# Kernel tuning notes

Hardware: AMD Instinct MI355X
Metric: run time of the kernel (lower is better)

The kernel has to match this reference:

```python
import jax, jax.numpy as jnp
import numpy as np

N, E, G = 50000, 500000, 8
IN, HID, OUT, NC, H = 256, 128, 64, 10, 2
NPG = N // G  # nodes per graph
NEG_SLOPE = 0.2


def setup_inputs() -> dict:
    key = jax.random.key(0)
    ks = jax.random.split(key, 24)
    x = jax.random.normal(ks[0], (N, IN), jnp.float32)
    # edges constrained to stay within each graph, no self-loops
    src = jax.random.randint(ks[1], (E,), 0, N)
    base = (src // NPG) * NPG
    off = jax.random.randint(ks[2], (E,), 1, NPG)
    dst = base + (src - base + off) % NPG
    edge_index = jnp.stack([src, dst], axis=0).astype(jnp.int32)
    edge_attr = jax.random.uniform(ks[3], (E, 1), jnp.float32)
    batch = jnp.repeat(jnp.arange(G, dtype=jnp.int32), NPG)
    y = jax.random.randint(ks[4], (N,), 0, NC).astype(jnp.int32)

    s = 0.1
    p = {
        'W1': jax.random.normal(ks[5], (IN, H * HID), jnp.float32) * s,
        'att_src1': jax.random.normal(ks[6], (H, HID), jnp.float32) * s,
        'att_dst1': jax.random.normal(ks[7], (H, HID), jnp.float32) * s,
        'We1': jax.random.normal(ks[8], (1, H * HID), jnp.float32) * s,
        'att_edge1': jax.random.normal(ks[9], (H, HID), jnp.float32) * s,
        'b1': jnp.zeros((HID,), jnp.float32),
        'W2': jax.random.normal(ks[10], (HID, H * OUT), jnp.float32) * s,
        'att_src2': jax.random.normal(ks[11], (H, OUT), jnp.float32) * s,
        'att_dst2': jax.random.normal(ks[12], (H, OUT), jnp.float32) * s,
        'We2': jax.random.normal(ks[13], (1, H * OUT), jnp.float32) * s,
        'att_edge2': jax.random.normal(ks[14], (H, OUT), jnp.float32) * s,
        'b2': jnp.zeros((OUT,), jnp.float32),
        'Wc': jax.random.normal(ks[15], (OUT, NC), jnp.float32) * s,
        'bc': jnp.zeros((NC,), jnp.float32),
    }
    return dict(x=x, edge_index=edge_index, edge_attr=edge_attr, batch=batch, y=y, **p)


def _gat_layer(x, src, dst, eattr, W, a_src, a_dst, We, a_e, b, n_nodes, C):
    # PyG GATConv: heads=H, concat=False (mean over heads), edge_dim features.
    xp = (x @ W).reshape(n_nodes, H, C)                    # [N,H,C]
    al_s = jnp.einsum('nhc,hc->nh', xp, a_src)             # [N,H]
    al_d = jnp.einsum('nhc,hc->nh', xp, a_dst)
    ef = (eattr @ We).reshape(-1, H, C)                    # [E,H,C]
    al_e = jnp.einsum('ehc,hc->eh', ef, a_e)               # [E,H]
    alpha = jax.nn.leaky_relu(al_s[src] + al_d[dst] + al_e, NEG_SLOPE)
    # edge softmax grouped by destination (every dst has a self-loop -> no empty segs)
    m = jax.ops.segment_max(alpha, dst, num_segments=n_nodes)
    ex = jnp.exp(alpha - m[dst])
    denom = jax.ops.segment_sum(ex, dst, num_segments=n_nodes)
    w = ex / (denom[dst] + 1e-16)                          # [E,H]
    msg = xp[src] * w[:, :, None]                          # [E,H,C]
    out = jax.ops.segment_sum(msg, dst, num_segments=n_nodes)  # [N,H,C]
    return out.mean(axis=1) + b


def reference(x, edge_index, edge_attr, batch, y,
              W1, att_src1, att_dst1, We1, att_edge1, b1,
              W2, att_src2, att_dst2, We2, att_edge2, b2,
              Wc, bc):
    src, dst = edge_index[0], edge_index[1]
    # add self-loops; edge_attr fill = per-graph mean (as in the per-graph loop)
    g = batch[src]
    cnt = jax.ops.segment_sum(jnp.ones_like(edge_attr[:, 0]), g, num_segments=G)
    mean_attr = jax.ops.segment_sum(edge_attr, g, num_segments=G) / cnt[:, None]
    loop_attr = mean_attr[batch]                           # [N,1]
    ar = jnp.arange(N, dtype=src.dtype)
    src_a = jnp.concatenate([src, ar])
    dst_a = jnp.concatenate([dst, ar])
    ea = jnp.concatenate([edge_attr, loop_attr], axis=0)

    h = _gat_layer(x, src_a, dst_a, ea, W1, att_src1, att_dst1, We1, att_edge1, b1, N, HID)
    h = jax.nn.relu(h)
    h = _gat_layer(h, src_a, dst_a, ea, W2, att_src2, att_dst2, We2, att_edge2, b2, N, OUT)
    pred = h @ Wc + bc                                     # [N,NC]
    return pred, y
```

## Files before the change

kernel.cpp:

```cpp
#include <hip/hip_runtime.h>
#include <hip/hip_bf16.h>
#include <cstdint>
#include <cstddef>

#define N_NODES 50000
#define N_EDGES 500000
#define EA_EDGES 550000
#define NPG 6250
#define G_GRAPHS 8
#define IN_DIM 256
#define HID_DIM 128
#define OUT_DIM 64
#define NCLS 10
#define NEG_SLOPE 0.2f

typedef __attribute__((ext_vector_type(8))) short short8v;
typedef __attribute__((ext_vector_type(4))) float f32x4;

__device__ __forceinline__ unsigned short f2bf(float f) {
  __hip_bfloat16 h = __float2bfloat16(f);
  unsigned short u;
  __builtin_memcpy(&u, &h, 2);
  return u;
}
__device__ __forceinline__ float bf2f(unsigned short u) {
  return __uint_as_float(((unsigned)u) << 16);
}

__global__ void k_graph_sums(const int* __restrict__ src, const float* __restrict__ eattr,
                             float* __restrict__ sums, float* __restrict__ cnts) {
  __shared__ float ls[G_GRAPHS], lc[G_GRAPHS];
  if (threadIdx.x < G_GRAPHS) { ls[threadIdx.x] = 0.f; lc[threadIdx.x] = 0.f; }
  __syncthreads();
  int stride = gridDim.x * blockDim.x;
  for (int e = blockIdx.x * blockDim.x + threadIdx.x; e < N_EDGES; e += stride) {
    int g = src[e] / NPG;
    atomicAdd(&ls[g], eattr[e]);
    atomicAdd(&lc[g], 1.f);
  }
  __syncthreads();
  if (threadIdx.x < G_GRAPHS) {
    atomicAdd(&sums[threadIdx.x], ls[threadIdx.x]);
    atomicAdd(&cnts[threadIdx.x], lc[threadIdx.x]);
  }
}

__global__ void k_prep(const float* __restrict__ sums, const float* __restrict__ cnts,
                       float* __restrict__ mean,
                       const float* __restrict__ We1, const float* __restrict__ ae1,
                       const float* __restrict__ We2, const float* __restrict__ ae2,
                       float* __restrict__ ce) {
  if (threadIdx.x == 0 && blockIdx.x == 0) {
    for (int g = 0; g < G_GRAPHS; ++g) mean[g] = sums[g] / cnts[g];
    for (int h = 0; h < 2; ++h) {
      float s = 0.f;
      for (int c = 0; c < HID_DIM; ++c) s += We1[h * HID_DIM + c] * ae1[h * HID_DIM + c];
      ce[h] = s;
    }
    for (int h = 0; h < 2; ++h) {
      float s = 0.f;
      for (int c = 0; c < OUT_DIM; ++c) s += We2[h * OUT_DIM + c] * ae2[h * OUT_DIM + c];
      ce[2 + h] = s;
    }
  }
}

__global__ void k_degree(const int* __restrict__ dst, int* __restrict__ deg) {
  int e = blockIdx.x * blockDim.x + threadIdx.x;
  if (e >= EA_EDGES) return;
  int d = (e < N_EDGES) ? dst[e] : (e - N_EDGES);
  atomicAdd(&deg[d], 1);
}

__global__ void k_scan1(const int* __restrict__ deg, int* __restrict__ rowptr,
                        int* __restrict__ bsum, int n) {
  __shared__ int sm[1024];
  int tid = threadIdx.x;
  int i = blockIdx.x * 1024 + tid;
  int v = (i < n) ? deg[i] : 0;
  sm[tid] = v;
  __syncthreads();
  for (int off = 1; off < 1024; off <<= 1) {
    int t = (tid >= off) ? sm[tid - off] : 0;
    __syncthreads();
    if (tid >= off) sm[tid] += t;
    __syncthreads();
  }
  if (i < n) rowptr[i] = sm[tid] - v;
  if (tid == 1023) bsum[blockIdx.x] = sm[1023];
}

__global__ void k_scan2(int* __restrict__ bsum, int* __restrict__ rowptr, int nb, int n) {
  if (threadIdx.x == 0 && blockIdx.x == 0) {
    int run = 0;
    for (int i = 0; i < nb; ++i) { int v = bsum[i]; bsum[i] = run; run += v; }
    rowptr[n] = run;
  }
}

__global__ void k_scan3(int* __restrict__ rowptr, int* __restrict__ cursor,
                        const int* __restrict__ bsum, int n) {
  int i = blockIdx.x * blockDim.x + threadIdx.x;
  if (i < n) {
    int r = rowptr[i] + bsum[i >> 10];
    rowptr[i] = r;
    cursor[i] = r;
  }
}

__global__ void k_fill(const int* __restrict__ src, const int* __restrict__ dst,
                       const float* __restrict__ eattr, const float* __restrict__ mean,
                       int* __restrict__ cursor,
                       int* __restrict__ csr_src, float* __restrict__ csr_ea) {
  int e = blockIdx.x * blockDim.x + threadIdx.x;
  if (e >= EA_EDGES) return;
  int s, d; float a;
  if (e < N_EDGES) { s = src[e]; d = dst[e]; a = eattr[e]; }
  else { int i = e - N_EDGES; s = i; d = i; a = mean[i / NPG]; }
  int p = atomicAdd(&cursor[d], 1);
  csr_src[p] = s;
  csr_ea[p] = a;
}

__global__ void k_cast_bf16(const float* __restrict__ in, unsigned short* __restrict__ out, int n8) {
  int i = blockIdx.x * blockDim.x + threadIdx.x;
  if (i >= n8) return;
  float4 a = *(const float4*)(in + (size_t)i * 8);
  float4 b = *(const float4*)(in + (size_t)i * 8 + 4);
  uint4 o;
  o.x = (unsigned)f2bf(a.x) | ((unsigned)f2bf(a.y) << 16);
  o.y = (unsigned)f2bf(a.z) | ((unsigned)f2bf(a.w) << 16);
  o.z = (unsigned)f2bf(b.x) | ((unsigned)f2bf(b.y) << 16);
  o.w = (unsigned)f2bf(b.z) | ((unsigned)f2bf(b.w) << 16);
  *(uint4*)(out + (size_t)i * 8) = o;
}

__global__ void k_cast_t(const float* __restrict__ W, unsigned short* __restrict__ Wt,
                         int K, int N) {
  int i = blockIdx.x * blockDim.x + threadIdx.x;
  if (i >= K * N) return;
  int k = i / N, n = i - k * N;
  Wt[(size_t)n * K + k] = f2bf(W[i]);
}

template <int K>
__global__ __launch_bounds__(256) void k_gemm_mfma(const unsigned short* __restrict__ A,
                                                   const unsigned short* __restrict__ Bt,
                                                   unsigned short* __restrict__ C,
                                                   int M, int Nout) {
  constexpr int BM = 128, BN = 128, BK = 64;
  __shared__ __attribute__((aligned(16))) unsigned short As[BM * BK];
  __shared__ __attribute__((aligned(16))) unsigned short Bs[BN * BK];
  const int tid = threadIdx.x;
  const int lane = tid & 63;
  const int wid = tid >> 6;
  const int wr = wid >> 1, wc = wid & 1;
  const int r0 = blockIdx.y * BM, c0 = blockIdx.x * BN;
  f32x4 acc[4][4] = {};

  for (int k0 = 0; k0 < K; k0 += BK) {
#pragma unroll
    for (int i = 0; i < 4; ++i) {
      int c = tid + i * 256;
      int row = c >> 3, kc = c & 7;
      int gr = r0 + row;
      uint4 v = make_uint4(0, 0, 0, 0);
      if (gr < M) v = *(const uint4*)(A + (size_t)gr * K + k0 + kc * 8);
      int boff = (row * 128 + kc * 16) ^ ((row & 7) << 4);
      *(uint4*)((char*)As + boff) = v;
    }
#pragma unroll
    for (int i = 0; i < 4; ++i) {
      int c = tid + i * 256;
      int row = c >> 3, kc = c & 7;
      uint4 v = *(const uint4*)(Bt + (size_t)(c0 + row) * K + k0 + kc * 8);
      int boff = (row * 128 + kc * 16) ^ ((row & 7) << 4);
      *(uint4*)((char*)Bs + boff) = v;
    }
    __syncthreads();
#pragma unroll
    for (int ks = 0; ks < 2; ++ks) {
      short8v a[4], b[4];
#pragma unroll
      for (int mi = 0; mi < 4; ++mi) {
        int row = wr * 64 + mi * 16 + (lane & 15);
        int boff = (row * 128 + ks * 64 + (lane >> 4) * 16) ^ ((row & 7) << 4);
        a[mi] = *(const short8v*)((const char*)As + boff);
      }
#pragma unroll
      for (int ni = 0; ni < 4; ++ni) {
        int row = wc * 64 + ni * 16 + (lane & 15);
        int boff = (row * 128 + ks * 64 + (lane >> 4) * 16) ^ ((row & 7) << 4);
        b[ni] = *(const short8v*)((const char*)Bs + boff);
      }
#pragma unroll
      for (int mi = 0; mi < 4; ++mi)
#pragma unroll
        for (int ni = 0; ni < 4; ++ni)
          acc[mi][ni] = __builtin_amdgcn_mfma_f32_16x16x32_bf16(a[mi], b[ni], acc[mi][ni], 0, 0, 0);
    }
    __syncthreads();
  }
#pragma unroll
  for (int mi = 0; mi < 4; ++mi) {
#pragma unroll
    for (int r = 0; r < 4; ++r) {
      int row = r0 + wr * 64 + mi * 16 + (lane >> 4) * 4 + r;
      if (row < M) {
#pragma unroll
        for (int ni = 0; ni < 4; ++ni) {
          int col = c0 + wc * 64 + ni * 16 + (lane & 15);
          C[(size_t)row * Nout + col] = f2bf(acc[mi][ni][r]);
        }
      }
    }
  }
}

template <int C>
__global__ void k_als(const unsigned short* __restrict__ xp, const float* __restrict__ a_src,
                      const float* __restrict__ a_dst, float* __restrict__ als,
                      float* __restrict__ ald) {
  constexpr int TC = 2 * C;
  constexpr int VPL = TC / 64;
  int wave = (blockIdx.x * blockDim.x + threadIdx.x) >> 6;
  int lane = threadIdx.x & 63;
  if (wave >= N_NODES) return;
  const unsigned short* row = xp + (size_t)wave * TC + lane * VPL;
  float v[VPL];
  if (VPL == 4) {
    ushort4 u = *(const ushort4*)row;
    v[0] = bf2f(u.x); v[1] = bf2f(u.y); v[2] = bf2f(u.z); v[3] = bf2f(u.w);
  } else {
    ushort2 u = *(const ushort2*)row;
    v[0] = bf2f(u.x); v[1] = bf2f(u.y);
  }
  float s_ = 0.f, d_ = 0.f;
#pragma unroll
  for (int k = 0; k < VPL; ++k) {
    s_ += v[k] * a_src[lane * VPL + k];
    d_ += v[k] * a_dst[lane * VPL + k];
  }
#pragma unroll
  for (int off = 1; off < 32; off <<= 1) {
    s_ += __shfl_xor(s_, off);
    d_ += __shfl_xor(d_, off);
  }
  if (lane == 0)  { als[2 * wave]     = s_; ald[2 * wave]     = d_; }
  if (lane == 32) { als[2 * wave + 1] = s_; ald[2 * wave + 1] = d_; }
}

template <int C, bool RELU, bool BF16OUT>
__global__ void k_aggregate(const unsigned short* __restrict__ xp,
                            const float* __restrict__ als, const float* __restrict__ ald,
                            const int* __restrict__ rowptr, const int* __restrict__ csr_src,
                            const float* __restrict__ csr_ea, const float* __restrict__ ce,
                            const float* __restrict__ bias, void* __restrict__ outv) {
  constexpr int TC = 2 * C;
  constexpr int VPL = TC / 64;
  int lane = threadIdx.x & 63;
  int wid = threadIdx.x >> 6;
  int local = (blockIdx.x >> 3) * 4 + wid;
  if (local >= NPG) return;
  int node = (blockIdx.x & 7) * NPG + local;
  int p0 = rowptr[node], p1 = rowptr[node + 1];
  int myh = lane >> 5;
  float ald_m = ald[2 * node + myh];
  float ce_m = ce[myh];
  float m = -1e30f, den = 0.f;
  float acc[VPL];
#pragma unroll
  for (int k = 0; k < VPL; ++k) acc[k] = 0.f;
  for (int p = p0; p < p1; ++p) {
    int s = csr_src[p];
    float ea = csr_ea[p];
    float a = als[2 * s + myh] + ald_m + ce_m * ea;
    a = (a > 0.f) ? a : NEG_SLOPE * a;
    float nm = fmaxf(m, a);
    float cs = __expf(m - nm);
    float w = __expf(a - nm);
    m = nm;
    den = den * cs + w;
    const unsigned short* row = xp + (size_t)s * TC + lane * VPL;
    if (VPL == 4) {
      ushort4 u = *(const ushort4*)row;
      acc[0] = acc[0] * cs + w * bf2f(u.x);
      acc[1] = acc[1] * cs + w * bf2f(u.y);
      acc[2] = acc[2] * cs + w * bf2f(u.z);
      acc[3] = acc[3] * cs + w * bf2f(u.w);
    } else {
      ushort2 u = *(const ushort2*)row;
      acc[0] = acc[0] * cs + w * bf2f(u.x);
      acc[1] = acc[1] * cs + w * bf2f(u.y);
    }
  }
  float deni = 1.f / (den + 1e-16f);
  float t[VPL];
#pragma unroll
  for (int k = 0; k < VPL; ++k) {
    t[k] = acc[k] * deni;
    t[k] += __shfl_xor(t[k], 32);
  }
  if (lane < 32) {
    int c = lane * VPL;
    float v[VPL];
#pragma unroll
    for (int k = 0; k < VPL; ++k) {
      v[k] = 0.5f * t[k] + bias[c + k];
      if (RELU) v[k] = fmaxf(v[k], 0.f);
    }
    if (BF16OUT) {
      unsigned short* o = (unsigned short*)outv + (size_t)node * C + c;
      if (VPL == 4) {
        ushort4 u;
        u.x = f2bf(v[0]); u.y = f2bf(v[1]); u.z = f2bf(v[2]); u.w = f2bf(v[3]);
        *(ushort4*)o = u;
      } else {
        ushort2 u; u.x = f2bf(v[0]); u.y = f2bf(v[1]);
        *(ushort2*)o = u;
      }
    } else {
      float* o = (float*)outv + (size_t)node * C + c;
#pragma unroll
      for (int k = 0; k < VPL; ++k) o[k] = v[k];
    }
  }
}

__global__ void k_classifier(const float* __restrict__ h2, const float* __restrict__ Wc,
                             const float* __restrict__ bc, const int* __restrict__ y,
                             float* __restrict__ out) {
  __shared__ float wcs[OUT_DIM * NCLS];
  __shared__ float bcs[NCLS];
  for (int i = threadIdx.x; i < OUT_DIM * NCLS; i += blockDim.x) wcs[i] = Wc[i];
  if (threadIdx.x < NCLS) bcs[threadIdx.x] = bc[threadIdx.x];
  __syncthreads();
  int n = blockIdx.x * blockDim.x + threadIdx.x;
  if (n >= N_NODES) return;
  float acc[NCLS];
#pragma unroll
  for (int j = 0; j < NCLS; ++j) acc[j] = bcs[j];
  for (int k = 0; k < OUT_DIM; ++k) {
    float v = h2[(size_t)n * OUT_DIM + k];
#pragma unroll
    for (int j = 0; j < NCLS; ++j) acc[j] += v * wcs[k * NCLS + j];
  }
#pragma unroll
  for (int j = 0; j < NCLS; ++j) out[(size_t)n * NCLS + j] = acc[j];
  out[(size_t)N_NODES * NCLS + n] = (float)y[n];
}

extern "C" void kernel_launch(void* const* d_in, const int* in_sizes, int n_in,
                              void* d_out, int out_size, void* d_ws, size_t ws_size,
                              hipStream_t stream) {
  const float* x     = (const float*)d_in[0];
  const int*   ei    = (const int*)d_in[1];
  const float* eattr = (const float*)d_in[2];
  const int*   y     = (const int*)d_in[4];
  const float* W1  = (const float*)d_in[5];
  const float* as1 = (const float*)d_in[6];
  const float* ad1 = (const float*)d_in[7];
  const float* We1 = (const float*)d_in[8];
  const float* ae1 = (const float*)d_in[9];
  const float* b1  = (const float*)d_in[10];
  const float* W2  = (const float*)d_in[11];
  const float* as2 = (const float*)d_in[12];
  const float* ad2 = (const float*)d_in[13];
  const float* We2 = (const float*)d_in[14];
  const float* ae2 = (const float*)d_in[15];
  const float* b2  = (const float*)d_in[16];
  const float* Wc  = (const float*)d_in[17];
  const float* bc  = (const float*)d_in[18];
  float* out = (float*)d_out;

  const int* src = ei;
  const int* dst = ei + N_EDGES;

  char* wsb = (char*)d_ws;
  size_t o = 0;
  auto alloc = [&](size_t bytes) { size_t r = o; o = (o + bytes + 255) & ~(size_t)255; return r; };
  size_t o_sums   = alloc(G_GRAPHS * 4);
  size_t o_cnts   = alloc(G_GRAPHS * 4);
  size_t o_mean   = alloc(G_GRAPHS * 4);
  size_t o_ce     = alloc(4 * 4);
  size_t o_bsum   = alloc(64 * 4);
  size_t o_deg    = alloc((size_t)N_NODES * 4);
  size_t o_rowptr = alloc((size_t)(N_NODES + 1) * 4);
  size_t o_cursor = alloc((size_t)N_NODES * 4);
  size_t o_csrs   = alloc((size_t)EA_EDGES * 4);
  size_t o_csrea  = alloc((size_t)EA_EDGES * 4);
  size_t o_xb     = alloc((size_t)N_NODES * IN_DIM * 2);
  size_t o_wt1    = alloc((size_t)IN_DIM * 256 * 2);
  size_t o_wt2    = alloc((size_t)HID_DIM * 128 * 2);
  size_t o_xp     = alloc((size_t)N_NODES * 256 * 2);
  size_t o_h1b    = alloc((size_t)N_NODES * HID_DIM * 2);
  size_t o_h2     = alloc((size_t)N_NODES * OUT_DIM * 4);
  size_t o_als    = alloc((size_t)N_NODES * 2 * 4);
  size_t o_ald    = alloc((size_t)N_NODES * 2 * 4);
  (void)ws_size;

  float* sums   = (float*)(wsb + o_sums);
  float* mean   = (float*)(wsb + o_mean);
  float* ce     = (float*)(wsb + o_ce);
  int*   bsum   = (int*)(wsb + o_bsum);
  int*   deg    = (int*)(wsb + o_deg);
  int*   rowptr = (int*)(wsb + o_rowptr);
  int*   cursor = (int*)(wsb + o_cursor);
  int*   csrs   = (int*)(wsb + o_csrs);
  float* csrea  = (float*)(wsb + o_csrea);
  unsigned short* xb  = (unsigned short*)(wsb + o_xb);
  unsigned short* wt1 = (unsigned short*)(wsb + o_wt1);
  unsigned short* wt2 = (unsigned short*)(wsb + o_wt2);
  unsigned short* xp  = (unsigned short*)(wsb + o_xp);
  unsigned short* h1b = (unsigned short*)(wsb + o_h1b);
  float* h2     = (float*)(wsb + o_h2);
  float* als    = (float*)(wsb + o_als);
  float* ald    = (float*)(wsb + o_ald);
  float* cnts   = (float*)(wsb + o_cnts);

  hipMemsetAsync(sums, 0, G_GRAPHS * 4 * 2, stream);
  hipMemsetAsync(deg, 0, (size_t)N_NODES * 4, stream);

  k_cast_bf16<<<(N_NODES * IN_DIM / 8 + 255) / 256, 256, 0, stream>>>(x, xb, N_NODES * IN_DIM / 8);
  k_cast_t<<<(IN_DIM * 256 + 255) / 256, 256, 0, stream>>>(W1, wt1, IN_DIM, 256);
  k_cast_t<<<(HID_DIM * 128 + 255) / 256, 256, 0, stream>>>(W2, wt2, HID_DIM, 128);

  k_graph_sums<<<256, 256, 0, stream>>>(src, eattr, sums, cnts);
  k_prep<<<1, 64, 0, stream>>>(sums, cnts, mean, We1, ae1, We2, ae2, ce);

  int eaBlocks = (EA_EDGES + 255) / 256;
  k_degree<<<eaBlocks, 256, 0, stream>>>(dst, deg);
  int nScanBlocks = (N_NODES + 1023) / 1024;
  k_scan1<<<nScanBlocks, 1024, 0, stream>>>(deg, rowptr, bsum, N_NODES);
  k_scan2<<<1, 64, 0, stream>>>(bsum, rowptr, nScanBlocks, N_NODES);
  k_scan3<<<(N_NODES + 255) / 256, 256, 0, stream>>>(rowptr, cursor, bsum, N_NODES);
  k_fill<<<eaBlocks, 256, 0, stream>>>(src, dst, eattr, mean, cursor, csrs, csrea);

  int aggBlocks = G_GRAPHS * ((NPG + 3) / 4);

  {
    dim3 grid(256 / 128, (N_NODES + 127) / 128);
    k_gemm_mfma<IN_DIM><<<grid, 256, 0, stream>>>(xb, wt1, xp, N_NODES, 256);
  }
  k_als<HID_DIM><<<(N_NODES + 3) / 4, 256, 0, stream>>>(xp, as1, ad1, als, ald);
  k_aggregate<HID_DIM, true, true><<<aggBlocks, 256, 0, stream>>>(
      xp, als, ald, rowptr, csrs, csrea, ce, b1, h1b);

  {
    dim3 grid(128 / 128, (N_NODES + 127) / 128);
    k_gemm_mfma<HID_DIM><<<grid, 256, 0, stream>>>(h1b, wt2, xp, N_NODES, 128);
  }
  k_als<OUT_DIM><<<(N_NODES + 3) / 4, 256, 0, stream>>>(xp, as2, ad2, als, ald);
  k_aggregate<OUT_DIM, false, false><<<aggBlocks, 256, 0, stream>>>(
      xp, als, ald, rowptr, csrs, csrea, ce + 2, b2, h2);

  k_classifier<<<(N_NODES + 255) / 256, 256, 0, stream>>>(h2, Wc, bc, y, out);
}
```

Before: 380.8 us.

## Batch edge softmax across lanes in aggregation, pack CSR, fuse degree count

The aggregation kernel now processes a node's incoming edges in chunks of 32. Each lane loads one edge's metadata and computes its attention logit in parallel, and a warp-wide max and sum give an online softmax per chunk. Neighbour rows are then gathered in a broadcast loop with no rescaling per edge. The CSR source index and edge attribute are packed into one int2 array, and the degree counting kernel is merged into the graph-sum kernel. This removes the serial per-edge exp/max chain and the separate metadata loads, at the cost of extra shuffles, which are wasteful for low-degree nodes (about 11 edges on average).

Measured after the change: 340.9 us. 10.5% less time.

```diff
diff --git a/kernel.cpp b/kernel.cpp
--- a/kernel.cpp
+++ b/kernel.cpp
@@ -27,16 +27,23 @@
   return __uint_as_float(((unsigned)u) << 16);
 }
 
-__global__ void k_graph_sums(const int* __restrict__ src, const float* __restrict__ eattr,
-                             float* __restrict__ sums, float* __restrict__ cnts) {
+__global__ void k_sums_degree(const int* __restrict__ src, const int* __restrict__ dst,
+                              const float* __restrict__ eattr,
+                              float* __restrict__ sums, float* __restrict__ cnts,
+                              int* __restrict__ deg) {
   __shared__ float ls[G_GRAPHS], lc[G_GRAPHS];
   if (threadIdx.x < G_GRAPHS) { ls[threadIdx.x] = 0.f; lc[threadIdx.x] = 0.f; }
   __syncthreads();
   int stride = gridDim.x * blockDim.x;
-  for (int e = blockIdx.x * blockDim.x + threadIdx.x; e < N_EDGES; e += stride) {
-    int g = src[e] / NPG;
-    atomicAdd(&ls[g], eattr[e]);
-    atomicAdd(&lc[g], 1.f);
+  for (int e = blockIdx.x * blockDim.x + threadIdx.x; e < EA_EDGES; e += stride) {
+    if (e < N_EDGES) {
+      int g = src[e] / NPG;
+      atomicAdd(&ls[g], eattr[e]);
+      atomicAdd(&lc[g], 1.f);
+      atomicAdd(&deg[dst[e]], 1);
+    } else {
+      atomicAdd(&deg[e - N_EDGES], 1);
+    }
   }
   __syncthreads();
   if (threadIdx.x < G_GRAPHS) {
@@ -63,13 +70,6 @@
       ce[2 + h] = s;
     }
   }
-}
-
-__global__ void k_degree(const int* __restrict__ dst, int* __restrict__ deg) {
-  int e = blockIdx.x * blockDim.x + threadIdx.x;
-  if (e >= EA_EDGES) return;
-  int d = (e < N_EDGES) ? dst[e] : (e - N_EDGES);
-  atomicAdd(&deg[d], 1);
 }
 
 __global__ void k_scan1(const int* __restrict__ deg, int* __restrict__ rowptr,
@@ -110,16 +110,14 @@
 
 __global__ void k_fill(const int* __restrict__ src, const int* __restrict__ dst,
                        const float* __restrict__ eattr, const float* __restrict__ mean,
-                       int* __restrict__ cursor,
-                       int* __restrict__ csr_src, float* __restrict__ csr_ea) {
+                       int* __restrict__ cursor, int2* __restrict__ csr) {
   int e = blockIdx.x * blockDim.x + threadIdx.x;
   if (e >= EA_EDGES) return;
   int s, d; float a;
   if (e < N_EDGES) { s = src[e]; d = dst[e]; a = eattr[e]; }
   else { int i = e - N_EDGES; s = i; d = i; a = mean[i / NPG]; }
   int p = atomicAdd(&cursor[d], 1);
-  csr_src[p] = s;
-  csr_ea[p] = a;
+  csr[p] = make_int2(s, __float_as_int(a));
 }
 
 __global__ void k_cast_bf16(const float* __restrict__ in, unsigned short* __restrict__ out, int n8) {
@@ -253,8 +251,8 @@
 template <int C, bool RELU, bool BF16OUT>
 __global__ void k_aggregate(const unsigned short* __restrict__ xp,
                             const float* __restrict__ als, const float* __restrict__ ald,
-                            const int* __restrict__ rowptr, const int* __restrict__ csr_src,
-                            const float* __restrict__ csr_ea, const float* __restrict__ ce,
+                            const int* __restrict__ rowptr, const int2* __restrict__ csr,
+                            const float* __restrict__ ce,
                             const float* __restrict__ bias, void* __restrict__ outv) {
   constexpr int TC = 2 * C;
   constexpr int VPL = TC / 64;
@@ -264,36 +262,58 @@
   if (local >= NPG) return;
   int node = (blockIdx.x & 7) * NPG + local;
   int p0 = rowptr[node], p1 = rowptr[node + 1];
-  int myh = lane >> 5;
-  float ald_m = ald[2 * node + myh];
-  float ce_m = ce[myh];
+  int deg = p1 - p0;
+  int half = lane >> 5;
+  int sub = lane & 31;
+  float ald_m = ald[2 * node + half];
+  float ce_m = ce[half];
   float m = -1e30f, den = 0.f;
   float acc[VPL];
 #pragma unroll
   for (int k = 0; k < VPL; ++k) acc[k] = 0.f;
-  for (int p = p0; p < p1; ++p) {
-    int s = csr_src[p];
-    float ea = csr_ea[p];
-    float a = als[2 * s + myh] + ald_m + ce_m * ea;
-    a = (a > 0.f) ? a : NEG_SLOPE * a;
-    float nm = fmaxf(m, a);
+
+  for (int base = 0; base < deg; base += 32) {
+    int nE = min(32, deg - base);
+    float a = -1e30f;
+    int s = 0;
+    if (sub < nE) {
+      int2 md = csr[p0 + base + sub];
+      s = md.x;
+      float ea = __int_as_float(md.y);
+      float l = als[2 * s + half] + ald_m + ce_m * ea;
+      a = (l > 0.f) ? l : NEG_SLOPE * l;
+    }
+    float cm = a;
+#pragma unroll
+    for (int off = 1; off < 32; off <<= 1) cm = fmaxf(cm, __shfl_xor(cm, off));
+    float nm = fmaxf(m, cm);
     float cs = __expf(m - nm);
-    float w = __expf(a - nm);
     m = nm;
-    den = den * cs + w;
-    const unsigned short* row = xp + (size_t)s * TC + lane * VPL;
-    if (VPL == 4) {
-      ushort4 u = *(const ushort4*)row;
-      acc[0] = acc[0] * cs + w * bf2f(u.x);
-      acc[1] = acc[1] * cs + w * bf2f(u.y);
-      acc[2] = acc[2] * cs + w * bf2f(u.z);
-      acc[3] = acc[3] * cs + w * bf2f(u.w);
-    } else {
-      ushort2 u = *(const ushort2*)row;
-      acc[0] = acc[0] * cs + w * bf2f(u.x);
-      acc[1] = acc[1] * cs + w * bf2f(u.y);
-    }
-  }
+    float w = (sub < nE) ? __expf(a - m) : 0.f;
+    float ws = w;
+#pragma unroll
+    for (int off = 1; off < 32; off <<= 1) ws += __shfl_xor(ws, off);
+    den = den * cs + ws;
+#pragma unroll
+    for (int k = 0; k < VPL; ++k) acc[k] *= cs;
+    for (int e = 0; e < nE; ++e) {
+      int se = __shfl(s, e);
+      float wh = __shfl(w, e | (lane & 32));
+      const unsigned short* row = xp + (size_t)se * TC + lane * VPL;
+      if (VPL == 4) {
+        ushort4 u = *(const ushort4*)row;
+        acc[0] += wh * bf2f(u.x);
+        acc[1] += wh * bf2f(u.y);
+        acc[2] += wh * bf2f(u.z);
+        acc[3] += wh * bf2f(u.w);
+      } else {
+        ushort2 u = *(const ushort2*)row;
+        acc[0] += wh * bf2f(u.x);
+        acc[1] += wh * bf2f(u.y);
+      }
+    }
+  }
+
   float deni = 1.f / (den + 1e-16f);
   float t[VPL];
 #pragma unroll
@@ -387,8 +407,7 @@
   size_t o_deg    = alloc((size_t)N_NODES * 4);
   size_t o_rowptr = alloc((size_t)(N_NODES + 1) * 4);
   size_t o_cursor = alloc((size_t)N_NODES * 4);
-  size_t o_csrs   = alloc((size_t)EA_EDGES * 4);
-  size_t o_csrea  = alloc((size_t)EA_EDGES * 4);
+  size_t o_csr    = alloc((size_t)EA_EDGES * 8);
   size_t o_xb     = alloc((size_t)N_NODES * IN_DIM * 2);
   size_t o_wt1    = alloc((size_t)IN_DIM * 256 * 2);
   size_t o_wt2    = alloc((size_t)HID_DIM * 128 * 2);
@@ -400,14 +419,14 @@
   (void)ws_size;
 
   float* sums   = (float*)(wsb + o_sums);
+  float* cnts   = (float*)(wsb + o_cnts);
   float* mean   = (float*)(wsb + o_mean);
   float* ce     = (float*)(wsb + o_ce);
   int*   bsum   = (int*)(wsb + o_bsum);
   int*   deg    = (int*)(wsb + o_deg);
   int*   rowptr = (int*)(wsb + o_rowptr);
   int*   cursor = (int*)(wsb + o_cursor);
-  int*   csrs   = (int*)(wsb + o_csrs);
-  float* csrea  = (float*)(wsb + o_csrea);
+  int2*  csr    = (int2*)(wsb + o_csr);
   unsigned short* xb  = (unsigned short*)(wsb + o_xb);
   unsigned short* wt1 = (unsigned short*)(wsb + o_wt1);
   unsigned short* wt2 = (unsigned short*)(wsb + o_wt2);
@@ -416,7 +435,6 @@
   float* h2     = (float*)(wsb + o_h2);
   float* als    = (float*)(wsb + o_als);
   float* ald    = (float*)(wsb + o_ald);
-  float* cnts   = (float*)(wsb + o_cnts);
 
   hipMemsetAsync(sums, 0, G_GRAPHS * 4 * 2, stream);
   hipMemsetAsync(deg, 0, (size_t)N_NODES * 4, stream);
@@ -425,16 +443,15 @@
   k_cast_t<<<(IN_DIM * 256 + 255) / 256, 256, 0, stream>>>(W1, wt1, IN_DIM, 256);
   k_cast_t<<<(HID_DIM * 128 + 255) / 256, 256, 0, stream>>>(W2, wt2, HID_DIM, 128);
 
-  k_graph_sums<<<256, 256, 0, stream>>>(src, eattr, sums, cnts);
+  k_sums_degree<<<512, 256, 0, stream>>>(src, dst, eattr, sums, cnts, deg);
   k_prep<<<1, 64, 0, stream>>>(sums, cnts, mean, We1, ae1, We2, ae2, ce);
 
   int eaBlocks = (EA_EDGES + 255) / 256;
-  k_degree<<<eaBlocks, 256, 0, stream>>>(dst, deg);
   int nScanBlocks = (N_NODES + 1023) / 1024;
   k_scan1<<<nScanBlocks, 1024, 0, stream>>>(deg, rowptr, bsum, N_NODES);
   k_scan2<<<1, 64, 0, stream>>>(bsum, rowptr, nScanBlocks, N_NODES);
   k_scan3<<<(N_NODES + 255) / 256, 256, 0, stream>>>(rowptr, cursor, bsum, N_NODES);
-  k_fill<<<eaBlocks, 256, 0, stream>>>(src, dst, eattr, mean, cursor, csrs, csrea);
+  k_fill<<<eaBlocks, 256, 0, stream>>>(src, dst, eattr, mean, cursor, csr);
 
   int aggBlocks = G_GRAPHS * ((NPG + 3) / 4);
 
@@ -444,7 +461,7 @@
   }
   k_als<HID_DIM><<<(N_NODES + 3) / 4, 256, 0, stream>>>(xp, as1, ad1, als, ald);
   k_aggregate<HID_DIM, true, true><<<aggBlocks, 256, 0, stream>>>(
-      xp, als, ald, rowptr, csrs, csrea, ce, b1, h1b);
+      xp, als, ald, rowptr, csr, ce, b1, h1b);
 
   {
     dim3 grid(128 / 128, (N_NODES + 127) / 128);
@@ -452,7 +469,7 @@
   }
   k_als<OUT_DIM><<<(N_NODES + 3) / 4, 256, 0, stream>>>(xp, as2, ad2, als, ald);
   k_aggregate<OUT_DIM, false, false><<<aggBlocks, 256, 0, stream>>>(
-      xp, als, ald, rowptr, csrs, csrea, ce + 2, b2, h2);
+      xp, als, ald, rowptr, csr, ce + 2, b2, h2);
 
   k_classifier<<<(N_NODES + 255) / 256, 256, 0, stream>>>(h2, Wc, bc, y, out);
 }
```
